# Optimization experiments

Hardware: AMD Instinct MI355X
Metric: run time of the kernel (lower is better)

## Reference

```python
import jax, jax.numpy as jnp
import numpy as np

H = 8      # heads
D = 64     # dim_head
DIM = 512  # model dim (== H*D)
LN_EPS = 1e-5


def setup_inputs() -> dict:
    key = jax.random.key(0)
    ks = jax.random.split(key, 4)
    B, N = 8, 1024
    x = jax.random.normal(ks[0], (B, N, DIM), dtype=jnp.float32)
    # params (torch Linear y = x @ W^T; we store W already transposed as (in, out))
    w_qkv = jax.random.normal(ks[1], (DIM, 3 * H * D), dtype=jnp.float32) * (DIM ** -0.5)
    w_out = jax.random.normal(ks[2], (H * D, DIM), dtype=jnp.float32) * ((H * D) ** -0.5)
    b_out = jnp.zeros((DIM,), dtype=jnp.float32)
    ln_g = jnp.ones((DIM,), dtype=jnp.float32)
    ln_b = jnp.zeros((DIM,), dtype=jnp.float32)
    return {"x": x, "w_qkv": w_qkv, "w_out": w_out, "b_out": b_out,
            "ln_g": ln_g, "ln_b": ln_b}


def reference(x, w_qkv, w_out, b_out, ln_g, ln_b):
    b, n, _ = x.shape
    qkv = x @ w_qkv                                   # [b, n, 3*H*D]
    q, k, v = jnp.split(qkv, 3, axis=-1)              # each [b, n, H*D]

    def to_heads(t):                                  # 'b n (h d) -> (b h) n d'
        return t.reshape(b, n, H, D).transpose(0, 2, 1, 3).reshape(b * H, n, D)

    q = to_heads(q)
    k = to_heads(k)
    v = to_heads(v)

    # FAITHFUL to source: k.view(b*h, -1, n) is a row-major reshape, NOT a
    # transpose, and NO scale is applied (self.scale is unused in forward).
    k_r = k.reshape(b * H, D, n)                      # [(bh), D, n] reinterpreted
    dots = jnp.matmul(q, k_r)                          # [(bh), n, n]
    attn = jax.nn.softmax(dots, axis=-1)
    out = jnp.matmul(attn, v)                          # [(bh), n, D]

    # '(b h) n d -> b n (h d)'
    out = out.reshape(b, H, n, D).transpose(0, 2, 1, 3).reshape(b, n, H * D)
    out = out @ w_out + b_out                          # to_out Linear (dropout=0)

    mu = jnp.mean(out, axis=-1, keepdims=True)
    var = jnp.var(out, axis=-1, keepdims=True)
    out = (out - mu) * jax.lax.rsqrt(var + LN_EPS) * ln_g + ln_b
    return out + x
```

## Files before the change

kernel.cpp:

```cpp
#include <hip/hip_runtime.h>

typedef unsigned short u16;
typedef unsigned int u32;
typedef __attribute__((ext_vector_type(4))) float f32x4;
typedef __attribute__((ext_vector_type(8))) short s16x8;

__device__ __forceinline__ u16 bf16_rne(float f) {
    u32 u = __float_as_uint(f);
    u32 r = u + 0x7FFFu + ((u >> 16) & 1u);
    return (u16)(r >> 16);
}

__device__ __forceinline__ u32 cvt_pk_bf16(float lo, float hi) {
    u32 r;
    asm("v_cvt_pk_bf16_f32 %0, %1, %2" : "=v"(r) : "v"(lo), "v"(hi));
    return r;
}

__device__ __forceinline__ void gl_lds16(const void* g, void* l) {
    __builtin_amdgcn_global_load_lds(
        (const __attribute__((address_space(1))) u32*)g,
        (__attribute__((address_space(3))) u32*)l, 16, 0, 0);
}

#define MFMA16(a, b, c) __builtin_amdgcn_mfma_f32_16x16x32_bf16((a), (b), (c), 0, 0, 0)

__global__ __launch_bounds__(256) void k_prep(const float* __restrict__ x,
                                              const float* __restrict__ w_qkv,
                                              const float* __restrict__ w_out,
                                              u16* __restrict__ xbf,
                                              u16* __restrict__ wqkvt,
                                              u16* __restrict__ woutt) {
    const int tid = threadIdx.x;
    if (blockIdx.x < 4096) {
        int i = blockIdx.x * 256 + tid;
        f32x4 v = *(const f32x4*)(x + (size_t)i * 4);
        u32* p = (u32*)(xbf + (size_t)i * 4);
        p[0] = cvt_pk_bf16(v.x, v.y);
        p[1] = cvt_pk_bf16(v.z, v.w);
        return;
    }
    __shared__ float tile[32][33];
    int idx = blockIdx.x - 4096;
    int bx_lin = idx & 63, by4 = idx >> 6;
    const float* in;
    u16* out;
    int C, bxc;
    if (bx_lin < 48) { in = w_qkv; out = wqkvt; C = 1536; bxc = bx_lin; }
    else             { in = w_out; out = woutt; C = 512;  bxc = bx_lin - 48; }
    const int R = 512;
    int bx = bxc * 32;
    int by = by4 * 32;
    int tx = tid & 31;
    int ty = tid >> 5;
#pragma unroll
    for (int i = 0; i < 32; i += 8)
        tile[ty + i][tx] = in[(size_t)(by + ty + i) * C + bx + tx];
    __syncthreads();
#pragma unroll
    for (int i = 0; i < 32; i += 8)
        out[(size_t)(bx + ty + i) * R + by + tx] = bf16_rne(tile[tx][ty + i]);
}

__global__ __launch_bounds__(256) void k_qkv_gemm(
    const u16* __restrict__ xbf, const u16* __restrict__ wt,
    u16* __restrict__ qh, u16* __restrict__ kRT, u16* __restrict__ vT) {
    __shared__ __align__(16) u16 lA[2][128 * 64];
    __shared__ __align__(16) u16 lB[2][128 * 64];
    const int tid = threadIdx.x;
    const int lane = tid & 63, l15 = lane & 15, l4 = lane >> 4;
    const int wid = tid >> 6, wm = wid >> 1, wn = wid & 1;
    const int hw = blockIdx.x;
    const int e = hw & 7, idx = hw >> 3;
    const int m0 = (e + 8 * (idx / 12)) * 128;
    const int c0 = (idx % 12) * 128;

    const char* gA = (const char*)xbf + (size_t)m0 * 1024;
    const char* gB = (const char*)wt + (size_t)c0 * 1024;
    const int srow = tid >> 3;
    const int scol = (tid & 7) * 16;

    const f32x4 z4 = {0.f, 0.f, 0.f, 0.f};
    f32x4 acc[4][4];
#pragma unroll
    for (int i = 0; i < 4; ++i)
#pragma unroll
        for (int j = 0; j < 4; ++j) acc[i][j] = z4;

    auto stage = [&](int buf, int kt) {
#pragma unroll
        for (int q = 0; q < 4; ++q) {
            int row = q * 32 + srow;
            int sc = scol ^ ((row & 7) << 4);
            gl_lds16(gA + (size_t)row * 1024 + kt * 128 + sc,
                     (char*)lA[buf] + q * 4096 + tid * 16);
            gl_lds16(gB + (size_t)row * 1024 + kt * 128 + sc,
                     (char*)lB[buf] + q * 4096 + tid * 16);
        }
    };

    stage(0, 0);
    __syncthreads();
    for (int kt = 0; kt < 8; ++kt) {
        int buf = kt & 1;
        if (kt < 7) stage(buf ^ 1, kt + 1);
        s16x8 af[4][2], bfr[4][2];
#pragma unroll
        for (int i = 0; i < 4; ++i)
#pragma unroll
            for (int k2 = 0; k2 < 2; ++k2) {
                int ra = wm * 64 + i * 16 + l15;
                int ca = (k2 * 64 + l4 * 16) ^ ((ra & 7) << 4);
                af[i][k2] = *(const s16x8*)((const char*)lA[buf] + ra * 128 + ca);
                int rb = wn * 64 + i * 16 + l15;
                int cb = (k2 * 64 + l4 * 16) ^ ((rb & 7) << 4);
                bfr[i][k2] = *(const s16x8*)((const char*)lB[buf] + rb * 128 + cb);
            }
        __builtin_amdgcn_s_setprio(1);
#pragma unroll
        for (int i = 0; i < 4; ++i)
#pragma unroll
            for (int j = 0; j < 4; ++j)
#pragma unroll
                for (int k2 = 0; k2 < 2; ++k2)
                    acc[i][j] = MFMA16(af[i][k2], bfr[j][k2], acc[i][j]);
        __builtin_amdgcn_s_setprio(0);
        __syncthreads();
    }

    char* ct = (char*)lA;
    const int which = c0 >> 9;
    const int hb = (c0 & 511) >> 6;
    const int b = m0 >> 10;
    const int n0 = m0 & 1023;
    const int i4 = (m0 >> 7) & 7;

    if (which != 2) {
#pragma unroll
        for (int i = 0; i < 4; ++i)
#pragma unroll
            for (int j = 0; j < 4; ++j) {
                int col = wn * 64 + j * 16 + l15;
#pragma unroll
                for (int r = 0; r < 4; ++r) {
                    int rr = wm * 64 + i * 16 + l4 * 4 + r;
                    *(u16*)(ct + rr * 256 + ((col * 2) ^ ((rr & 7) << 4))) =
                        bf16_rne(acc[i][j][r]);
                }
            }
    } else {
#pragma unroll
        for (int i = 0; i < 4; ++i)
#pragma unroll
            for (int j = 0; j < 4; ++j) {
                int col = wn * 64 + j * 16 + l15;
#pragma unroll
                for (int r = 0; r < 4; ++r) {
                    int rr = wm * 64 + i * 16 + l4 * 4 + r;
                    *(u16*)(ct + col * 256 + ((rr * 2) ^ ((col & 7) << 4))) =
                        bf16_rne(acc[i][j][r]);
                }
            }
    }
    __syncthreads();

    if (which == 0) {
#pragma unroll
        for (int p = 0; p < 8; ++p) {
            int cid = p * 256 + tid;
            int row = cid >> 4, sub = cid & 15;
            s16x8 v = *(const s16x8*)(ct + row * 256 + ((sub * 16) ^ ((row & 7) << 4)));
            int bh = b * 8 + hb + (sub >> 3);
            *(s16x8*)((char*)qh + ((size_t)bh * 1024 + n0 + row) * 128 +
                      (sub & 7) * 16) = v;
        }
    } else if (which == 1) {
#pragma unroll
        for (int p = 0; p < 8; ++p) {
            int cid = p * 256 + tid;
            int h = cid >> 10, jb = (cid >> 6) & 15, jd = cid & 63;
            int colb = ((h * 64 + jd) * 2) ^ ((jb & 7) << 4);
            s16x8 v;
#pragma unroll
            for (int ii = 0; ii < 8; ++ii)
                v[ii] = *(const short*)(ct + (jb + ii * 16) * 256 + colb);
            int bh = b * 8 + hb + h;
            *(s16x8*)((char*)kRT + (size_t)bh * 131072 + jb * 8192 + i4 * 1024 +
                      jd * 16) = v;
        }
    } else {
#pragma unroll
        for (int p = 0; p < 8; ++p) {
            int cid = p * 256 + tid;
            int cl = cid >> 4, nc = cid & 15;
            s16x8 v = *(const s16x8*)(ct + cl * 256 + ((nc * 16) ^ ((cl & 7) << 4)));
            int bh = b * 8 + hb + (cl >> 6);
            *(s16x8*)((char*)vT + ((size_t)bh * 64 + (cl & 63)) * 2048 + n0 * 2 +
                      nc * 16) = v;
        }
    }
}

__global__ __launch_bounds__(256) void k_attn(
    const u16* __restrict__ qh, const u16* __restrict__ kRT,
    const u16* __restrict__ vT, u16* __restrict__ attn_out) {
    __shared__ __align__(16) char smem[49152];
    char* qtile = smem;
    char* ktb = smem + 16384;
    char* vtb = smem + 32768;

    const int tid = threadIdx.x;
    const int lane = tid & 63, l15 = lane & 15, l4 = lane >> 4;
    const int wid = tid >> 6;
    const int bh = blockIdx.x, mt = blockIdx.y;

    const char* kb = (const char*)kRT + (size_t)bh * 131072;
    const char* vb = (const char*)vT + (size_t)bh * 64 * 2048;
    const int srow = tid >> 3;
    const int scol = (tid & 7) * 16;

    {
        const char* gq = (const char*)qh + ((size_t)bh * 1024 + mt * 128) * 128;
#pragma unroll
        for (int q = 0; q < 4; ++q) {
            int row = q * 32 + srow;
            int sc = scol ^ ((row & 7) << 4);
            gl_lds16(gq + (size_t)row * 128 + sc, qtile + q * 4096 + tid * 16);
        }
#pragma unroll
        for (int q = 0; q < 2; ++q) {
            int jd = q * 32 + srow;
            int i4s = (tid & 7) ^ (jd & 7);
            gl_lds16(kb + i4s * 1024 + jd * 16, ktb + q * 4096 + tid * 16);
            int sc = scol ^ ((jd & 7) << 4);
            gl_lds16(vb + (size_t)jd * 2048 + sc, vtb + q * 4096 + tid * 16);
        }
    }
    __syncthreads();

    s16x8 qf[2][2];
#pragma unroll
    for (int m2 = 0; m2 < 2; ++m2)
#pragma unroll
        for (int k2 = 0; k2 < 2; ++k2) {
            int row = wid * 32 + m2 * 16 + l15;
            int cq = (k2 * 64 + l4 * 16) ^ ((row & 7) << 4);
            qf[m2][k2] = *(const s16x8*)(qtile + row * 128 + cq);
        }
    __syncthreads();

    char* ptw = smem + wid * 4096;

    const f32x4 z4 = {0.f, 0.f, 0.f, 0.f};
    f32x4 o[2][4];
    float den[2] = {0.f, 0.f};
#pragma unroll
    for (int m2 = 0; m2 < 2; ++m2)
#pragma unroll
        for (int d4 = 0; d4 < 4; ++d4) o[m2][d4] = z4;
    const float LOG2E = 1.4426950408889634f;

    for (int jb = 0; jb < 16; ++jb) {
        const int buf = jb & 1;
        if (jb < 15) {
            int nb = jb + 1, bufn = buf ^ 1;
#pragma unroll
            for (int q = 0; q < 2; ++q) {
                int jd = q * 32 + srow;
                int i4s = (tid & 7) ^ (jd & 7);
                gl_lds16(kb + (size_t)nb * 8192 + i4s * 1024 + jd * 16,
                         ktb + bufn * 8192 + q * 4096 + tid * 16);
                int sc = scol ^ ((jd & 7) << 4);
                gl_lds16(vb + (size_t)jd * 2048 + nb * 128 + sc,
                         vtb + bufn * 8192 + q * 4096 + tid * 16);
            }
        }
        const char* kt = ktb + buf * 8192;
        const char* vt = vtb + buf * 8192;

        s16x8 bk[4][2];
#pragma unroll
        for (int n4 = 0; n4 < 4; ++n4)
#pragma unroll
            for (int k2 = 0; k2 < 2; ++k2) {
                int rn = n4 * 16 + l15;
                int cb = (k2 * 64 + l4 * 16) ^ ((rn & 7) << 4);
                bk[n4][k2] = *(const s16x8*)(kt + rn * 128 + cb);
            }
        f32x4 s[2][4];
        __builtin_amdgcn_s_setprio(1);
#pragma unroll
        for (int m2 = 0; m2 < 2; ++m2)
#pragma unroll
            for (int n4 = 0; n4 < 4; ++n4) {
                s[m2][n4] = z4;
#pragma unroll
                for (int k2 = 0; k2 < 2; ++k2)
                    s[m2][n4] = MFMA16(bk[n4][k2], qf[m2][k2], s[m2][n4]);
            }
        __builtin_amdgcn_s_setprio(0);

#pragma unroll
        for (int m2 = 0; m2 < 2; ++m2) {
            int rloc = m2 * 16 + l15;
#pragma unroll
            for (int n4 = 0; n4 < 4; ++n4) {
                float e0 = exp2f(s[m2][n4][0] * LOG2E);
                float e1 = exp2f(s[m2][n4][1] * LOG2E);
                float e2 = exp2f(s[m2][n4][2] * LOG2E);
                float e3 = exp2f(s[m2][n4][3] * LOG2E);
                den[m2] += (e0 + e1) + (e2 + e3);
                uint2 w;
                w.x = cvt_pk_bf16(e0, e1);
                w.y = cvt_pk_bf16(e2, e3);
                *(uint2*)(ptw + rloc * 128 +
                          ((n4 * 32 + l4 * 8) ^ ((rloc & 7) << 4))) = w;
            }
        }

        s16x8 bv[4][2];
#pragma unroll
        for (int d4 = 0; d4 < 4; ++d4)
#pragma unroll
            for (int k2 = 0; k2 < 2; ++k2) {
                int rn = d4 * 16 + l15;
                int cb = (k2 * 64 + l4 * 16) ^ ((rn & 7) << 4);
                bv[d4][k2] = *(const s16x8*)(vt + rn * 128 + cb);
            }

        s16x8 pa[2][2];
#pragma unroll
        for (int m2 = 0; m2 < 2; ++m2) {
            int rloc = m2 * 16 + l15;
#pragma unroll
            for (int k2 = 0; k2 < 2; ++k2)
                pa[m2][k2] = *(const s16x8*)(ptw + rloc * 128 +
                                             ((k2 * 64 + l4 * 16) ^ ((rloc & 7) << 4)));
        }

        __builtin_amdgcn_s_setprio(1);
#pragma unroll
        for (int m2 = 0; m2 < 2; ++m2)
#pragma unroll
            for (int d4 = 0; d4 < 4; ++d4)
#pragma unroll
                for (int k2 = 0; k2 < 2; ++k2)
                    o[m2][d4] = MFMA16(bv[d4][k2], pa[m2][k2], o[m2][d4]);
        __builtin_amdgcn_s_setprio(0);

        if (jb < 15) __syncthreads();
    }

#pragma unroll
    for (int m2 = 0; m2 < 2; ++m2) {
        den[m2] += __shfl_xor(den[m2], 16);
        den[m2] += __shfl_xor(den[m2], 32);
    }

#pragma unroll
    for (int m2 = 0; m2 < 2; ++m2) {
        float inv = 1.0f / den[m2];
        int row = wid * 32 + m2 * 16 + l15;
        char* ow = smem + row * 128;
#pragma unroll
        for (int d4 = 0; d4 < 4; ++d4) {
            uint2 w;
            w.x = cvt_pk_bf16(o[m2][d4][0] * inv, o[m2][d4][1] * inv);
            w.y = cvt_pk_bf16(o[m2][d4][2] * inv, o[m2][d4][3] * inv);
            *(uint2*)(ow + ((d4 * 32 + l4 * 8) ^ ((row & 7) << 4))) = w;
        }
    }
    __syncthreads();

    {
        char* dst = (char*)attn_out + ((size_t)(bh >> 3) * 1024 + mt * 128) * 1024 +
                    (bh & 7) * 128;
#pragma unroll
        for (int p = 0; p < 4; ++p) {
            int cid = p * 256 + tid;
            int row = cid >> 3, sub = cid & 7;
            s16x8 v = *(const s16x8*)(smem + row * 128 +
                                      ((sub * 16) ^ ((row & 7) << 4)));
            *(s16x8*)(dst + (size_t)row * 1024 + sub * 16) = v;
        }
    }
}

__global__ __launch_bounds__(512) void k_out_ln(
    const u16* __restrict__ aout, const u16* __restrict__ wt,
    const float* __restrict__ bias, const float* __restrict__ x,
    const float* __restrict__ g, const float* __restrict__ bb,
    float* __restrict__ out) {
    __shared__ __align__(16) char smem[131072];
    char* lB[2] = {smem, smem + 65536};
    const int tid = threadIdx.x;
    const int lane = tid & 63, l15 = lane & 15, l4 = lane >> 4;
    const int wid = tid >> 6, wm = wid >> 2, wn = wid & 3;
    const int m0 = blockIdx.x * 32;

    s16x8 af[16];
    {
        const char* arow = (const char*)aout + (size_t)(m0 + wm * 16 + l15) * 1024;
#pragma unroll
        for (int kk = 0; kk < 16; ++kk)
            af[kk] = *(const s16x8*)(arow + kk * 64 + l4 * 16);
    }

    auto stageB = [&](int buf, int kt) {
#pragma unroll
        for (int p = 0; p < 8; ++p) {
            int cid = p * 512 + tid;
            int n = cid >> 3, cc = cid & 7;
            int sc = (cc * 16) ^ ((n & 7) << 4);
            gl_lds16((const char*)wt + (size_t)n * 1024 + kt * 128 + sc,
                     lB[buf] + cid * 16);
        }
    };

    const f32x4 z4 = {0.f, 0.f, 0.f, 0.f};
    f32x4 acc[8];
#pragma unroll
    for (int j = 0; j < 8; ++j) acc[j] = z4;

    stageB(0, 0);
    __syncthreads();
    for (int kt = 0; kt < 8; ++kt) {
        int buf = kt & 1;
        if (kt < 7) stageB(buf ^ 1, kt + 1);
        s16x8 bf2[8][2];
#pragma unroll
        for (int j = 0; j < 8; ++j)
#pragma unroll
            for (int q = 0; q < 2; ++q) {
                int n = wn * 128 + j * 16 + l15;
                int cb = (q * 64 + l4 * 16) ^ ((n & 7) << 4);
                bf2[j][q] = *(const s16x8*)(lB[buf] + n * 128 + cb);
            }
        __builtin_amdgcn_s_setprio(1);
#pragma unroll
        for (int j = 0; j < 8; ++j)
#pragma unroll
            for (int q = 0; q < 2; ++q)
                acc[j] = MFMA16(af[kt * 2 + q], bf2[j][q], acc[j]);
        __builtin_amdgcn_s_setprio(0);
        __syncthreads();
    }

#pragma unroll
    for (int j = 0; j < 8; ++j) {
        int col = wn * 128 + j * 16 + l15;
        float bo = bias[col];
#pragma unroll
        for (int r = 0; r < 4; ++r) {
            int row = wm * 16 + l4 * 4 + r;
            *(float*)(smem + row * 2048 + ((col * 4) ^ ((row & 7) << 4))) =
                acc[j][r] + bo;
        }
    }
    __syncthreads();

    f32x4 g0 = *(const f32x4*)(g + lane * 8);
    f32x4 g1 = *(const f32x4*)(g + lane * 8 + 4);
    f32x4 b0 = *(const f32x4*)(bb + lane * 8);
    f32x4 b1 = *(const f32x4*)(bb + lane * 8 + 4);
#pragma unroll
    for (int rr = 0; rr < 4; ++rr) {
        int row = wid * 4 + rr;
        int sw = (row & 7) << 4;
        f32x4 v0 = *(const f32x4*)(smem + row * 2048 + ((lane * 32) ^ sw));
        f32x4 v1 = *(const f32x4*)(smem + row * 2048 + ((lane * 32 + 16) ^ sw));
        float s = v0.x + v0.y + v0.z + v0.w + v1.x + v1.y + v1.z + v1.w;
        float sq = v0.x * v0.x + v0.y * v0.y + v0.z * v0.z + v0.w * v0.w +
                   v1.x * v1.x + v1.y * v1.y + v1.z * v1.z + v1.w * v1.w;
#pragma unroll
        for (int m = 1; m < 64; m <<= 1) {
            s += __shfl_xor(s, m);
            sq += __shfl_xor(sq, m);
        }
        float mu = s * (1.0f / 512.0f);
        float var = sq * (1.0f / 512.0f) - mu * mu;
        float rstd = rsqrtf(var + 1e-5f);

        const float* xr = x + (size_t)(m0 + row) * 512 + lane * 8;
        f32x4 x0 = *(const f32x4*)(xr);
        f32x4 x1 = *(const f32x4*)(xr + 4);
        f32x4 r0, r1;
#pragma unroll
        for (int u = 0; u < 4; ++u) {
            r0[u] = (v0[u] - mu) * rstd * g0[u] + b0[u] + x0[u];
            r1[u] = (v1[u] - mu) * rstd * g1[u] + b1[u] + x1[u];
        }
        float* orow = out + (size_t)(m0 + row) * 512 + lane * 8;
        *(f32x4*)(orow) = r0;
        *(f32x4*)(orow + 4) = r1;
    }
}

extern "C" void kernel_launch(void* const* d_in, const int* in_sizes, int n_in,
                              void* d_out, int out_size, void* d_ws, size_t ws_size,
                              hipStream_t stream) {
    const float* x = (const float*)d_in[0];
    const float* w_qkv = (const float*)d_in[1];
    const float* w_out = (const float*)d_in[2];
    const float* b_out = (const float*)d_in[3];
    const float* ln_g = (const float*)d_in[4];
    const float* ln_b = (const float*)d_in[5];
    float* out = (float*)d_out;
    char* ws = (char*)d_ws;

    u16* xbf = (u16*)(ws + 0);
    u16* wqkvt = (u16*)(ws + 8388608);
    u16* woutt = (u16*)(ws + 9961472);
    u16* qh = (u16*)(ws + 10485760);
    u16* kRT = (u16*)(ws + 18874368);
    u16* vT = (u16*)(ws + 27262976);
    u16* aout = (u16*)(ws + 35651584);

    k_prep<<<5120, 256, 0, stream>>>(x, w_qkv, w_out, xbf, wqkvt, woutt);
    k_qkv_gemm<<<768, 256, 0, stream>>>(xbf, wqkvt, qh, kRT, vT);
    k_attn<<<dim3(64, 8), 256, 0, stream>>>(qh, kRT, vT, aout);
    k_out_ln<<<256, 512, 0, stream>>>(aout, woutt, b_out, x, ln_g, ln_b, out);
}
```

Baseline: 85.25 us.

## Halve attention query tile to 64 rows and fold log2e into Q

The attention kernel now processes 64 query rows per block instead of 128. Each wave handles 16 rows, and the grid doubles to 64x16 blocks, which raises parallelism and occupancy through smaller LDS use and fewer registers. The log2(e) factor is folded into Q when the QKV GEMM writes it out, so the softmax exp2 no longer needs a multiply. In exchange, K/V tiles are loaded twice as often in total, and rounding Q to bf16 after scaling changes numerics slightly.

```diff
diff --git a/kernel.cpp b/kernel.cpp
--- a/kernel.cpp
+++ b/kernel.cpp
@@ -134,6 +134,7 @@
     const int b = m0 >> 10;
     const int n0 = m0 & 1023;
     const int i4 = (m0 >> 7) & 7;
+    const float qsc = (which == 0) ? 1.4426950408889634f : 1.0f;
 
     if (which != 2) {
 #pragma unroll
@@ -145,7 +146,7 @@
                 for (int r = 0; r < 4; ++r) {
                     int rr = wm * 64 + i * 16 + l4 * 4 + r;
                     *(u16*)(ct + rr * 256 + ((col * 2) ^ ((rr & 7) << 4))) =
-                        bf16_rne(acc[i][j][r]);
+                        bf16_rne(acc[i][j][r] * qsc);
                 }
             }
     } else {
@@ -204,10 +205,10 @@
 __global__ __launch_bounds__(256) void k_attn(
     const u16* __restrict__ qh, const u16* __restrict__ kRT,
     const u16* __restrict__ vT, u16* __restrict__ attn_out) {
-    __shared__ __align__(16) char smem[49152];
+    __shared__ __align__(16) char smem[40960];
     char* qtile = smem;
-    char* ktb = smem + 16384;
-    char* vtb = smem + 32768;
+    char* ktb = smem + 8192;
+    char* vtb = smem + 24576;
 
     const int tid = threadIdx.x;
     const int lane = tid & 63, l15 = lane & 15, l4 = lane >> 4;
@@ -220,9 +221,9 @@
     const int scol = (tid & 7) * 16;
 
     {
-        const char* gq = (const char*)qh + ((size_t)bh * 1024 + mt * 128) * 128;
-#pragma unroll
-        for (int q = 0; q < 4; ++q) {
+        const char* gq = (const char*)qh + ((size_t)bh * 1024 + mt * 64) * 128;
+#pragma unroll
+        for (int q = 0; q < 2; ++q) {
             int row = q * 32 + srow;
             int sc = scol ^ ((row & 7) << 4);
             gl_lds16(gq + (size_t)row * 128 + sc, qtile + q * 4096 + tid * 16);
@@ -238,27 +239,22 @@
     }
     __syncthreads();
 
-    s16x8 qf[2][2];
-#pragma unroll
-    for (int m2 = 0; m2 < 2; ++m2)
-#pragma unroll
-        for (int k2 = 0; k2 < 2; ++k2) {
-            int row = wid * 32 + m2 * 16 + l15;
-            int cq = (k2 * 64 + l4 * 16) ^ ((row & 7) << 4);
-            qf[m2][k2] = *(const s16x8*)(qtile + row * 128 + cq);
-        }
-    __syncthreads();
-
-    char* ptw = smem + wid * 4096;
+    s16x8 qf[2];
+#pragma unroll
+    for (int k2 = 0; k2 < 2; ++k2) {
+        int row = wid * 16 + l15;
+        int cq = (k2 * 64 + l4 * 16) ^ ((row & 7) << 4);
+        qf[k2] = *(const s16x8*)(qtile + row * 128 + cq);
+    }
+    __syncthreads();
+
+    char* ptw = smem + wid * 2048;
 
     const f32x4 z4 = {0.f, 0.f, 0.f, 0.f};
-    f32x4 o[2][4];
-    float den[2] = {0.f, 0.f};
-#pragma unroll
-    for (int m2 = 0; m2 < 2; ++m2)
-#pragma unroll
-        for (int d4 = 0; d4 < 4; ++d4) o[m2][d4] = z4;
-    const float LOG2E = 1.4426950408889634f;
+    f32x4 o[4];
+    float den = 0.f;
+#pragma unroll
+    for (int d4 = 0; d4 < 4; ++d4) o[d4] = z4;
 
     for (int jb = 0; jb < 16; ++jb) {
         const int buf = jb & 1;
@@ -287,35 +283,29 @@
                 int cb = (k2 * 64 + l4 * 16) ^ ((rn & 7) << 4);
                 bk[n4][k2] = *(const s16x8*)(kt + rn * 128 + cb);
             }
-        f32x4 s[2][4];
+        f32x4 s[4];
         __builtin_amdgcn_s_setprio(1);
 #pragma unroll
-        for (int m2 = 0; m2 < 2; ++m2)
-#pragma unroll
-            for (int n4 = 0; n4 < 4; ++n4) {
-                s[m2][n4] = z4;
-#pragma unroll
-                for (int k2 = 0; k2 < 2; ++k2)
-                    s[m2][n4] = MFMA16(bk[n4][k2], qf[m2][k2], s[m2][n4]);
-            }
+        for (int n4 = 0; n4 < 4; ++n4) {
+            s[n4] = z4;
+#pragma unroll
+            for (int k2 = 0; k2 < 2; ++k2)
+                s[n4] = MFMA16(bk[n4][k2], qf[k2], s[n4]);
+        }
         __builtin_amdgcn_s_setprio(0);
 
 #pragma unroll
-        for (int m2 = 0; m2 < 2; ++m2) {
-            int rloc = m2 * 16 + l15;
-#pragma unroll
-            for (int n4 = 0; n4 < 4; ++n4) {
-                float e0 = exp2f(s[m2][n4][0] * LOG2E);
-                float e1 = exp2f(s[m2][n4][1] * LOG2E);
-                float e2 = exp2f(s[m2][n4][2] * LOG2E);
-                float e3 = exp2f(s[m2][n4][3] * LOG2E);
-                den[m2] += (e0 + e1) + (e2 + e3);
-                uint2 w;
-                w.x = cvt_pk_bf16(e0, e1);
-                w.y = cvt_pk_bf16(e2, e3);
-                *(uint2*)(ptw + rloc * 128 +
-                          ((n4 * 32 + l4 * 8) ^ ((rloc & 7) << 4))) = w;
-            }
+        for (int n4 = 0; n4 < 4; ++n4) {
+            float e0 = exp2f(s[n4][0]);
+            float e1 = exp2f(s[n4][1]);
+            float e2 = exp2f(s[n4][2]);
+            float e3 = exp2f(s[n4][3]);
+            den += (e0 + e1) + (e2 + e3);
+            uint2 w;
+            w.x = cvt_pk_bf16(e0, e1);
+            w.y = cvt_pk_bf16(e2, e3);
+            *(uint2*)(ptw + l15 * 128 +
+                      ((n4 * 32 + l4 * 8) ^ ((l15 & 7) << 4))) = w;
         }
 
         s16x8 bv[4][2];
@@ -328,55 +318,45 @@
                 bv[d4][k2] = *(const s16x8*)(vt + rn * 128 + cb);
             }
 
-        s16x8 pa[2][2];
-#pragma unroll
-        for (int m2 = 0; m2 < 2; ++m2) {
-            int rloc = m2 * 16 + l15;
+        s16x8 pa[2];
+#pragma unroll
+        for (int k2 = 0; k2 < 2; ++k2)
+            pa[k2] = *(const s16x8*)(ptw + l15 * 128 +
+                                     ((k2 * 64 + l4 * 16) ^ ((l15 & 7) << 4)));
+
+        __builtin_amdgcn_s_setprio(1);
+#pragma unroll
+        for (int d4 = 0; d4 < 4; ++d4)
 #pragma unroll
             for (int k2 = 0; k2 < 2; ++k2)
-                pa[m2][k2] = *(const s16x8*)(ptw + rloc * 128 +
-                                             ((k2 * 64 + l4 * 16) ^ ((rloc & 7) << 4)));
-        }
-
-        __builtin_amdgcn_s_setprio(1);
-#pragma unroll
-        for (int m2 = 0; m2 < 2; ++m2)
-#pragma unroll
-            for (int d4 = 0; d4 < 4; ++d4)
-#pragma unroll
-                for (int k2 = 0; k2 < 2; ++k2)
-                    o[m2][d4] = MFMA16(bv[d4][k2], pa[m2][k2], o[m2][d4]);
+                o[d4] = MFMA16(bv[d4][k2], pa[k2], o[d4]);
         __builtin_amdgcn_s_setprio(0);
 
         if (jb < 15) __syncthreads();
     }
 
-#pragma unroll
-    for (int m2 = 0; m2 < 2; ++m2) {
-        den[m2] += __shfl_xor(den[m2], 16);
-        den[m2] += __shfl_xor(den[m2], 32);
-    }
-
-#pragma unroll
-    for (int m2 = 0; m2 < 2; ++m2) {
-        float inv = 1.0f / den[m2];
-        int row = wid * 32 + m2 * 16 + l15;
+    den += __shfl_xor(den, 16);
+    den += __shfl_xor(den, 32);
+    float inv = 1.0f / den;
+
+    {
+        int row = wid * 16 + l15;
         char* ow = smem + row * 128;
 #pragma unroll
         for (int d4 = 0; d4 < 4; ++d4) {
             uint2 w;
-            w.x = cvt_pk_bf16(o[m2][d4][0] * inv, o[m2][d4][1] * inv);
-            w.y = cvt_pk_bf16(o[m2][d4][2] * inv, o[m2][d4][3] * inv);
+            w.x = cvt_pk_bf16(o[d4][0] * inv, o[d4][1] * inv);
+            w.y = cvt_pk_bf16(o[d4][2] * inv, o[d4][3] * inv);
             *(uint2*)(ow + ((d4 * 32 + l4 * 8) ^ ((row & 7) << 4))) = w;
         }
     }
     __syncthreads();
 
     {
-        char* dst = (char*)attn_out + ((size_t)(bh >> 3) * 1024 + mt * 128) * 1024 +
+        char* dst = (char*)attn_out + ((size_t)(bh >> 3) * 1024 + mt * 64) * 1024 +
                     (bh & 7) * 128;
 #pragma unroll
-        for (int p = 0; p < 4; ++p) {
+        for (int p = 0; p < 2; ++p) {
             int cid = p * 256 + tid;
             int row = cid >> 3, sub = cid & 7;
             s16x8 v = *(const s16x8*)(smem + row * 128 +
@@ -518,6 +498,6 @@
 
     k_prep<<<5120, 256, 0, stream>>>(x, w_qkv, w_out, xbf, wqkvt, woutt);
     k_qkv_gemm<<<768, 256, 0, stream>>>(xbf, wqkvt, qh, kRT, vT);
-    k_attn<<<dim3(64, 8), 256, 0, stream>>>(qh, kRT, vT, aout);
+    k_attn<<<dim3(64, 16), 256, 0, stream>>>(qh, kRT, vT, aout);
     k_out_ln<<<256, 512, 0, stream>>>(aout, woutt, b_out, x, ln_g, ln_b, out);
 }
```

After: 82.54 us. 3.2% less time.
